# Kernel tuning notes

Hardware: AMD Instinct MI355X
Metric: run time of the kernel (lower is better)

The kernel has to match this reference:

```python
import jax, jax.numpy as jnp
import numpy as np

B, S, H, NH = 2, 2048, 1024, 16
DH = H // NH  # 64

def setup_inputs() -> dict:
    key = jax.random.key(0)
    ks = jax.random.split(key, 6)
    return {
        "hidden_states": jax.random.normal(ks[0], (B, S, H), jnp.float32),
        "attention_mask": jnp.zeros((B, 1, 1, S), jnp.float32),  # additive mask (0 = attend)
        "local_attention_mask": jax.random.randint(ks[1], (B, 1, S, S), 0, 2).astype(jnp.int32),
        "gate_outputs": jax.random.uniform(ks[2], (B, NH, S, 1), jnp.float32),
        "Wq": jax.random.normal(ks[3], (H, H), jnp.float32) * 0.02,
        "bq": jnp.zeros((H,), jnp.float32),
        "Wk": jax.random.normal(ks[4], (H, H), jnp.float32) * 0.02,
        "bk": jnp.zeros((H,), jnp.float32),
        "Wv": jax.random.normal(ks[5], (H, H), jnp.float32) * 0.02,
        "bv": jnp.zeros((H,), jnp.float32),
    }

def _heads(x):
    # [B,S,H] -> [B,NH,S,DH]
    return x.reshape(B, S, NH, DH).transpose(0, 2, 1, 3)

def reference(hidden_states, attention_mask, local_attention_mask, gate_outputs, Wq, bq, Wk, bk, Wv, bv):
    q = _heads(hidden_states @ Wq.T + bq)
    k = _heads(hidden_states @ Wk.T + bk)
    v = _heads(hidden_states @ Wv.T + bv)
    scores = jnp.einsum("bhqd,bhkd->bhqk", q, k) / jnp.sqrt(jnp.float32(DH))
    # global branch (additive mask)
    probs_g = jax.nn.softmax(scores + attention_mask, axis=-1)
    ctx_g = jnp.einsum("bhqk,bhkd->bhqd", probs_g, v)
    # local branch: 0/1 mask -> additive -inf mask
    lmask = (1.0 - local_attention_mask.astype(jnp.float32)) * jnp.finfo(jnp.float32).min
    probs_l = jax.nn.softmax(scores + lmask, axis=-1)
    ctx_l = jnp.einsum("bhqk,bhkd->bhqd", probs_l, v)
    ctx = gate_outputs * ctx_l + (1.0 - gate_outputs) * ctx_g  # [B,NH,S,DH]
    return ctx.transpose(0, 2, 1, 3).reshape(B, S, H)
```

## Files before the change

kernel.cpp:

```cpp
#include <hip/hip_runtime.h>
#include <cstdint>
#include <cstddef>

typedef short short8 __attribute__((ext_vector_type(8)));
typedef float floatx4 __attribute__((ext_vector_type(4)));
typedef unsigned short ushort4v __attribute__((ext_vector_type(4)));
typedef unsigned int uintx4 __attribute__((ext_vector_type(4)));

constexpr int B_ = 2, S_ = 2048, H_ = 1024, NH_ = 16, DH_ = 64;
constexpr int K_ = H_;

__device__ __forceinline__ unsigned short f2bf(float f) {
  unsigned u = __float_as_uint(f);
  u += 0x7fffu + ((u >> 16) & 1u);
  return (unsigned short)(u >> 16);
}

__device__ __forceinline__ unsigned cvtpk(float a, float b) {
  unsigned r;
  asm("v_cvt_pk_bf16_f32 %0, %1, %2" : "=v"(r) : "v"(a), "v"(b));
  return r;
}

__global__ __launch_bounds__(256) void prep_kernel(
    const float* __restrict__ hs, unsigned short* __restrict__ hbf,
    const float* __restrict__ Wq, const float* __restrict__ Wk, const float* __restrict__ Wv,
    unsigned short* __restrict__ wqb, unsigned short* __restrict__ wkb,
    unsigned short* __restrict__ wvb,
    const int* __restrict__ lm, unsigned long long* __restrict__ bm,
    const float* __restrict__ am, float* __restrict__ ea) {
  const int bid = blockIdx.x, tid = threadIdx.x;
  if (bid < 1792) {
    const float* in;
    unsigned short* out;
    int off;
    if (bid < 1024) { in = hs; out = hbf; off = bid; }
    else {
      int wsel = (bid - 1024) >> 8;
      in = (wsel == 0) ? Wq : (wsel == 1) ? Wk : Wv;
      out = (wsel == 0) ? wqb : (wsel == 1) ? wkb : wvb;
      off = (bid - 1024) & 255;
    }
    const int base = off * 4096;
#pragma unroll
    for (int j = 0; j < 4; j++) {
      int i = base + j * 1024 + tid * 4;
      float4 v = *reinterpret_cast<const float4*>(in + i);
      ushort4v o;
      o.x = f2bf(v.x); o.y = f2bf(v.y); o.z = f2bf(v.z); o.w = f2bf(v.w);
      *reinterpret_cast<ushort4v*>(out + i) = o;
    }
  } else if (bid < 9984) {
    const int wbase = (bid - 1792) * 16 + (tid >> 6) * 4;
    const int lane = tid & 63;
#pragma unroll
    for (int j = 0; j < 4; j++) {
      unsigned long long bits = __ballot(lm[(size_t)(wbase + j) * 64 + lane] != 0);
      if (lane == 0) bm[wbase + j] = bits;
    }
  } else {
#pragma unroll
    for (int j = 0; j < 4; j++) {
      int i = j * 1024 + tid * 4;
      float4 v = *reinterpret_cast<const float4*>(am + i);
      float4 o;
      o.x = __expf(v.x); o.y = __expf(v.y); o.z = __expf(v.z); o.w = __expf(v.w);
      *reinterpret_cast<float4*>(ea + i) = o;
    }
  }
}

typedef __attribute__((address_space(1))) const void gvoid;
typedef __attribute__((address_space(3))) void lvoid;
__device__ __forceinline__ void async16(const unsigned short* gp, unsigned short* lp) {
  __builtin_amdgcn_global_load_lds((gvoid*)gp, (lvoid*)lp, 16, 0, 0);
}

__global__ __launch_bounds__(256) void gemm_qkv(
    const unsigned short* __restrict__ A,
    const unsigned short* __restrict__ Wq, const unsigned short* __restrict__ Wk,
    const unsigned short* __restrict__ Wv,
    const float* __restrict__ bq, const float* __restrict__ bk, const float* __restrict__ bv,
    unsigned short* __restrict__ qo, unsigned short* __restrict__ ko,
    unsigned short* __restrict__ vo) {
  __shared__ alignas(16) unsigned short As[2][128 * 32];
  __shared__ alignas(16) unsigned short Bs[2][128 * 32];
  const int z = blockIdx.z;
  const unsigned short* W = (z == 0) ? Wq : (z == 1) ? Wk : Wv;
  const float* bias = (z == 0) ? bq : (z == 1) ? bk : bv;

  const int m0 = blockIdx.x * 128, n0 = blockIdx.y * 128;
  const int tid = threadIdx.x, lane = tid & 63, wvi = tid >> 6;
  const int wr = wvi >> 1, wc = wvi & 1, quad = lane >> 4, l16 = lane & 15;

  floatx4 zf = {0.f, 0.f, 0.f, 0.f};
  floatx4 acc[4][4];
  for (int i = 0; i < 4; i++)
    for (int j = 0; j < 4; j++) acc[i][j] = zf;

  const int cb0 = wvi * 128;
  const int cb1 = wvi * 128 + 64;
  const int c0 = cb0 + lane, c1 = cb1 + lane;
  const unsigned short* As0 = A + (size_t)(m0 + (c0 >> 2)) * K_ + (c0 & 3) * 8;
  const unsigned short* As1 = A + (size_t)(m0 + (c1 >> 2)) * K_ + (c1 & 3) * 8;
  const unsigned short* Ws0 = W + (size_t)(n0 + (c0 >> 2)) * K_ + (c0 & 3) * 8;
  const unsigned short* Ws1 = W + (size_t)(n0 + (c1 >> 2)) * K_ + (c1 & 3) * 8;

  async16(As0, &As[0][cb0 * 8]);
  async16(Ws0, &Bs[0][cb0 * 8]);
  async16(As1, &As[0][cb1 * 8]);
  async16(Ws1, &Bs[0][cb1 * 8]);
  __syncthreads();

  for (int kt = 0; kt < 32; kt++) {
    if (kt != 31) {
      const int kk = (kt + 1) * 32;
      const int bn = (kt + 1) & 1;
      async16(As0 + kk, &As[bn][cb0 * 8]);
      async16(Ws0 + kk, &Bs[bn][cb0 * 8]);
      async16(As1 + kk, &As[bn][cb1 * 8]);
      async16(Ws1 + kk, &Bs[bn][cb1 * 8]);
    }
    const unsigned short* Ah = As[kt & 1];
    const unsigned short* Bh = Bs[kt & 1];
    short8 af[4], bfr[4];
#pragma unroll
    for (int mf = 0; mf < 4; mf++)
      af[mf] = *reinterpret_cast<const short8*>(&Ah[(wr * 64 + mf * 16 + l16) * 32 + quad * 8]);
#pragma unroll
    for (int nf = 0; nf < 4; nf++)
      bfr[nf] = *reinterpret_cast<const short8*>(&Bh[(wc * 64 + nf * 16 + l16) * 32 + quad * 8]);
    if (z == 2) {
#pragma unroll
      for (int mf = 0; mf < 4; mf++)
#pragma unroll
        for (int nf = 0; nf < 4; nf++)
          acc[mf][nf] = __builtin_amdgcn_mfma_f32_16x16x32_bf16(af[mf], bfr[nf], acc[mf][nf], 0, 0, 0);
    } else {
#pragma unroll
      for (int mf = 0; mf < 4; mf++)
#pragma unroll
        for (int nf = 0; nf < 4; nf++)
          acc[mf][nf] = __builtin_amdgcn_mfma_f32_16x16x32_bf16(bfr[nf], af[mf], acc[mf][nf], 0, 0, 0);
    }
    __syncthreads();
  }

  if (z == 2) {
#pragma unroll
    for (int mf = 0; mf < 4; mf++) {
      int mbase = m0 + wr * 64 + mf * 16 + quad * 4;
      int b = mbase >> 11, s0 = mbase & 2047;
      int kl = s0 & 63;
#pragma unroll
      for (int nf = 0; nf < 4; nf++) {
        int n = n0 + wc * 64 + nf * 16 + l16;
        int h = n >> 6, d = n & 63;
        int bh = b * NH_ + h;
        float bvv = bias[n];
        floatx4 c = acc[mf][nf];
        size_t base = (size_t)bh * 131072 + (s0 >> 6) * 4096 + (d >> 4) * 1024 +
                      (kl >> 5) * 512 + ((kl >> 3) & 3) * 128 + (d & 15) * 8 + (kl & 7);
        ushort4v p;
        p.x = f2bf(c[0] + bvv); p.y = f2bf(c[1] + bvv);
        p.z = f2bf(c[2] + bvv); p.w = f2bf(c[3] + bvv);
        *reinterpret_cast<ushort4v*>(&vo[base]) = p;
      }
    }
  } else {
#pragma unroll
    for (int mf = 0; mf < 4; mf++) {
      int s = m0 + wr * 64 + mf * 16 + l16;
      int b = s >> 11;
      int sq = s & 2047;
#pragma unroll
      for (int nf = 0; nf < 4; nf++) {
        int nn = n0 + wc * 64 + nf * 16 + quad * 4;
        int h = nn >> 6, dh = nn & 63;
        int bh = b * NH_ + h;
        float4 b4 = *reinterpret_cast<const float4*>(bias + nn);
        floatx4 c = acc[mf][nf];
        if (z == 0) {
          ushort4v p;
          p.x = f2bf((c[0] + b4.x) * 0.18033688011112042f);
          p.y = f2bf((c[1] + b4.y) * 0.18033688011112042f);
          p.z = f2bf((c[2] + b4.z) * 0.18033688011112042f);
          p.w = f2bf((c[3] + b4.w) * 0.18033688011112042f);
          *reinterpret_cast<ushort4v*>(&qo[((size_t)bh * S_ + sq) * DH_ + dh]) = p;
        } else {
          int kl = sq & 63;
          int t = ((kl >> 4) & 2) | ((kl >> 2) & 1);
          int rr = ((kl >> 1) & 12) | (kl & 3);
          size_t base = (size_t)bh * 131072 + (sq >> 6) * 4096 + t * 1024 +
                        (dh >> 5) * 512 + ((dh >> 3) & 3) * 128 + rr * 8 + (dh & 7);
          ushort4v p;
          p.x = f2bf(c[0] + b4.x); p.y = f2bf(c[1] + b4.y);
          p.z = f2bf(c[2] + b4.z); p.w = f2bf(c[3] + b4.w);
          *reinterpret_cast<ushort4v*>(&ko[base]) = p;
        }
      }
    }
  }
}

__global__ __launch_bounds__(256, 4) void attn_kernel(
    const unsigned short* __restrict__ q,
    const unsigned short* __restrict__ kperm,
    const unsigned short* __restrict__ vperm,
    const float* __restrict__ eam,
    const unsigned long long* __restrict__ bm,
    const float* __restrict__ gate,
    float* __restrict__ out) {
  __shared__ alignas(16) unsigned short Ks[2][4096];
  __shared__ alignas(16) unsigned short Vs[2][4096];

  const int flat = blockIdx.x;
  const int h = (flat & 7) + 8 * ((flat >> 3) & 1);
  const int b = (flat >> 4) & 1;
  const int qt = flat >> 5;
  const int tid = threadIdx.x, lane = tid & 63, wvi = tid >> 6;
  const int quad = lane >> 4, l16 = lane & 15;
  const int bh = b * NH_ + h;
  const int q0 = qt * 64 + wvi * 16;
  const int quad8 = quad * 8;

  const unsigned short* qrow = q + ((size_t)bh * S_ + q0 + l16) * DH_;
  short8 qf0 = *reinterpret_cast<const short8*>(qrow + quad * 8);
  short8 qf1 = *reinterpret_cast<const short8*>(qrow + 32 + quad * 8);

  floatx4 zf = {0.f, 0.f, 0.f, 0.f};
  float psg = 0.f, psl = 0.f;
  floatx4 accg[4], accl[4];
#pragma unroll
  for (int i = 0; i < 4; i++) { accg[i] = zf; accl[i] = zf; }

  const unsigned short* kp = kperm + (size_t)bh * 131072;
  const unsigned short* vp = vperm + (size_t)bh * 131072;
  const float* eamb = eam + (size_t)b * S_;
  const unsigned long long* bmq = bm + ((size_t)b * S_ + q0 + l16) * (S_ / 64);

  const int soA = tid * 8, soB = 2048 + tid * 8;
  const unsigned short* kgA = kp + soA;
  const unsigned short* kgB = kp + soB;
  const unsigned short* vgA = vp + soA;
  const unsigned short* vgB = vp + soB;

  uint4 pk0 = *reinterpret_cast<const uint4*>(kgA);
  uint4 pk1 = *reinterpret_cast<const uint4*>(kgB);
  uint4 pv0 = *reinterpret_cast<const uint4*>(vgA);
  uint4 pv1 = *reinterpret_cast<const uint4*>(vgB);
  *reinterpret_cast<uint4*>(&Ks[0][soA]) = pk0;
  *reinterpret_cast<uint4*>(&Ks[0][soB]) = pk1;
  *reinterpret_cast<uint4*>(&Vs[0][soA]) = pv0;
  *reinterpret_cast<uint4*>(&Vs[0][soB]) = pv1;
  pk0 = *reinterpret_cast<const uint4*>(kgA + 4096);
  pk1 = *reinterpret_cast<const uint4*>(kgB + 4096);
  pv0 = *reinterpret_cast<const uint4*>(vgA + 4096);
  pv1 = *reinterpret_cast<const uint4*>(vgB + 4096);

  for (int kt = 0; kt < S_ / 64; kt++) {
    __syncthreads();
    {
      const int bn = (kt + 1) & 1;
      *reinterpret_cast<uint4*>(&Ks[bn][soA]) = pk0;
      *reinterpret_cast<uint4*>(&Ks[bn][soB]) = pk1;
      *reinterpret_cast<uint4*>(&Vs[bn][soA]) = pv0;
      *reinterpret_cast<uint4*>(&Vs[bn][soB]) = pv1;
    }
    {
      const int tb = ((kt + 2) & 31) * 4096;
      pk0 = *reinterpret_cast<const uint4*>(kgA + tb);
      pk1 = *reinterpret_cast<const uint4*>(kgB + tb);
      pv0 = *reinterpret_cast<const uint4*>(vgA + tb);
      pv1 = *reinterpret_cast<const uint4*>(vgB + tb);
    }
    const int k0 = kt * 64;
    uint2 wv = *reinterpret_cast<const uint2*>(&bmq[kt]);
    unsigned wq0 = wv.x >> quad8;
    unsigned wq1 = wv.y >> quad8;
    float4 ea0 = *reinterpret_cast<const float4*>(eamb + k0 + quad8);
    float4 ea1 = *reinterpret_cast<const float4*>(eamb + k0 + 4 + quad8);
    float4 ea2 = *reinterpret_cast<const float4*>(eamb + k0 + 32 + quad8);
    float4 ea3 = *reinterpret_cast<const float4*>(eamb + k0 + 36 + quad8);

    const unsigned short* Kc = Ks[kt & 1];
    const unsigned short* Vc = Vs[kt & 1];
    floatx4 scT[4];
#pragma unroll
    for (int t = 0; t < 4; t++) {
      const unsigned short* kr = Kc + t * 1024 + lane * 8;
      short8 kf0 = *reinterpret_cast<const short8*>(kr);
      short8 kf1 = *reinterpret_cast<const short8*>(kr + 512);
      scT[t] = __builtin_amdgcn_mfma_f32_16x16x32_bf16(kf0, qf0, zf, 0, 0, 0);
      scT[t] = __builtin_amdgcn_mfma_f32_16x16x32_bf16(kf1, qf1, scT[t], 0, 0, 0);
    }
    uintx4 fgv[2], flv[2];
#pragma unroll
    for (int t = 0; t < 4; t++) {
      const int T = t >> 1, tau = t & 1;
      floatx4 sc = scT[t];
      unsigned wq = T ? wq1 : wq0;
      float4 ea = (t == 0) ? ea0 : (t == 1) ? ea1 : (t == 2) ? ea2 : ea3;
      unsigned m4 = (wq >> (tau * 4)) & 0xFu;
      float e0 = __builtin_amdgcn_exp2f(sc[0]);
      float e1 = __builtin_amdgcn_exp2f(sc[1]);
      float e2 = __builtin_amdgcn_exp2f(sc[2]);
      float e3 = __builtin_amdgcn_exp2f(sc[3]);
      float g0 = e0 * ea.x, g1 = e1 * ea.y, g2 = e2 * ea.z, g3 = e3 * ea.w;
      psg += (g0 + g1) + (g2 + g3);
      float l0 = (m4 & 1u) ? e0 : 0.f;
      float l1 = (m4 & 2u) ? e1 : 0.f;
      float l2 = (m4 & 4u) ? e2 : 0.f;
      float l3 = (m4 & 8u) ? e3 : 0.f;
      psl += (l0 + l1) + (l2 + l3);
      fgv[T][tau * 2]     = cvtpk(g0, g1);
      fgv[T][tau * 2 + 1] = cvtpk(g2, g3);
      flv[T][tau * 2]     = cvtpk(l0, l1);
      flv[T][tau * 2 + 1] = cvtpk(l2, l3);
    }
    short8 FG0 = __builtin_bit_cast(short8, fgv[0]);
    short8 FG1 = __builtin_bit_cast(short8, fgv[1]);
    short8 FL0 = __builtin_bit_cast(short8, flv[0]);
    short8 FL1 = __builtin_bit_cast(short8, flv[1]);
#pragma unroll
    for (int d = 0; d < 4; d++) {
      const unsigned short* vb = Vc + d * 1024 + lane * 8;
      short8 v0 = *reinterpret_cast<const short8*>(vb);
      short8 v1 = *reinterpret_cast<const short8*>(vb + 512);
      accg[d] = __builtin_amdgcn_mfma_f32_16x16x32_bf16(v0, FG0, accg[d], 0, 0, 0);
      accl[d] = __builtin_amdgcn_mfma_f32_16x16x32_bf16(v0, FL0, accl[d], 0, 0, 0);
      accg[d] = __builtin_amdgcn_mfma_f32_16x16x32_bf16(v1, FG1, accg[d], 0, 0, 0);
      accl[d] = __builtin_amdgcn_mfma_f32_16x16x32_bf16(v1, FL1, accl[d], 0, 0, 0);
    }
  }

  float lgf = psg;
  lgf += __shfl_xor(lgf, 16, 64);
  lgf += __shfl_xor(lgf, 32, 64);
  float llf = psl;
  llf += __shfl_xor(llf, 16, 64);
  llf += __shfl_xor(llf, 32, 64);
  const int s = q0 + l16;
  const float g = gate[(size_t)bh * S_ + s];
  const float cg = (1.f - g) / lgf, cl = g / llf;
  float* orow = out + ((size_t)b * S_ + s) * H_ + h * DH_ + quad * 4;
#pragma unroll
  for (int d = 0; d < 4; d++) {
    float4 o;
    o.x = cl * accl[d][0] + cg * accg[d][0];
    o.y = cl * accl[d][1] + cg * accg[d][1];
    o.z = cl * accl[d][2] + cg * accg[d][2];
    o.w = cl * accl[d][3] + cg * accg[d][3];
    *reinterpret_cast<float4*>(orow + d * 16) = o;
  }
}

extern "C" void kernel_launch(void* const* d_in, const int* in_sizes, int n_in,
                              void* d_out, int out_size, void* d_ws, size_t ws_size,
                              hipStream_t stream) {
  (void)in_sizes; (void)n_in; (void)out_size; (void)ws_size;
  const float* hs = (const float*)d_in[0];
  const float* am = (const float*)d_in[1];
  const int* lm = (const int*)d_in[2];
  const float* gate = (const float*)d_in[3];
  const float* Wq = (const float*)d_in[4];
  const float* bq = (const float*)d_in[5];
  const float* Wk = (const float*)d_in[6];
  const float* bk = (const float*)d_in[7];
  const float* Wv = (const float*)d_in[8];
  const float* bv = (const float*)d_in[9];
  float* out = (float*)d_out;

  unsigned short* ws = (unsigned short*)d_ws;
  unsigned short* hbf = ws;
  unsigned short* wqb = hbf + 4194304;
  unsigned short* wkb = wqb + 1048576;
  unsigned short* wvb = wkb + 1048576;
  unsigned short* qb = wvb + 1048576;
  unsigned short* kb = qb + 4194304;
  unsigned short* vtb = kb + 4194304;
  unsigned long long* bmp = (unsigned long long*)(vtb + 4194304);
  float* eamp = (float*)(bmp + 131072);

  prep_kernel<<<9985, 256, 0, stream>>>(hs, hbf, Wq, Wk, Wv, wqb, wkb, wvb, lm, bmp, am, eamp);
  gemm_qkv<<<dim3(32, 8, 3), 256, 0, stream>>>(hbf, wqb, wkb, wvb, bq, bk, bv, qb, kb, vtb);
  attn_kernel<<<dim3(1024), 256, 0, stream>>>(qb, kb, vtb, eamp, bmp, gate, out);
}
```

Baseline: 234.5 us.

## Fuse fp32-to-bf16 conversion into QKV GEMM tile loads

Removes the separate bf16 conversion pass over hidden states and weights from the prep kernel. The GEMM now loads fp32 tiles directly into registers, converts them with packed bf16 instructions, and writes them to LDS, prefetching two tiles ahead in a register-staged pipeline instead of using async global-to-LDS loads. This drops a full write and re-read of the bf16 copies. In exchange the GEMM reads twice as many bytes per tile, each tile is converted by every block that uses it, and register pressure goes up.

```diff
diff --git a/kernel.cpp b/kernel.cpp
--- a/kernel.cpp
+++ b/kernel.cpp
@@ -23,35 +23,11 @@
 }
 
 __global__ __launch_bounds__(256) void prep_kernel(
-    const float* __restrict__ hs, unsigned short* __restrict__ hbf,
-    const float* __restrict__ Wq, const float* __restrict__ Wk, const float* __restrict__ Wv,
-    unsigned short* __restrict__ wqb, unsigned short* __restrict__ wkb,
-    unsigned short* __restrict__ wvb,
     const int* __restrict__ lm, unsigned long long* __restrict__ bm,
     const float* __restrict__ am, float* __restrict__ ea) {
   const int bid = blockIdx.x, tid = threadIdx.x;
-  if (bid < 1792) {
-    const float* in;
-    unsigned short* out;
-    int off;
-    if (bid < 1024) { in = hs; out = hbf; off = bid; }
-    else {
-      int wsel = (bid - 1024) >> 8;
-      in = (wsel == 0) ? Wq : (wsel == 1) ? Wk : Wv;
-      out = (wsel == 0) ? wqb : (wsel == 1) ? wkb : wvb;
-      off = (bid - 1024) & 255;
-    }
-    const int base = off * 4096;
-#pragma unroll
-    for (int j = 0; j < 4; j++) {
-      int i = base + j * 1024 + tid * 4;
-      float4 v = *reinterpret_cast<const float4*>(in + i);
-      ushort4v o;
-      o.x = f2bf(v.x); o.y = f2bf(v.y); o.z = f2bf(v.z); o.w = f2bf(v.w);
-      *reinterpret_cast<ushort4v*>(out + i) = o;
-    }
-  } else if (bid < 9984) {
-    const int wbase = (bid - 1792) * 16 + (tid >> 6) * 4;
+  if (bid < 8192) {
+    const int wbase = bid * 16 + (tid >> 6) * 4;
     const int lane = tid & 63;
 #pragma unroll
     for (int j = 0; j < 4; j++) {
@@ -70,23 +46,17 @@
   }
 }
 
-typedef __attribute__((address_space(1))) const void gvoid;
-typedef __attribute__((address_space(3))) void lvoid;
-__device__ __forceinline__ void async16(const unsigned short* gp, unsigned short* lp) {
-  __builtin_amdgcn_global_load_lds((gvoid*)gp, (lvoid*)lp, 16, 0, 0);
-}
-
 __global__ __launch_bounds__(256) void gemm_qkv(
-    const unsigned short* __restrict__ A,
-    const unsigned short* __restrict__ Wq, const unsigned short* __restrict__ Wk,
-    const unsigned short* __restrict__ Wv,
+    const float* __restrict__ A,
+    const float* __restrict__ Wq, const float* __restrict__ Wk,
+    const float* __restrict__ Wv,
     const float* __restrict__ bq, const float* __restrict__ bk, const float* __restrict__ bv,
     unsigned short* __restrict__ qo, unsigned short* __restrict__ ko,
     unsigned short* __restrict__ vo) {
   __shared__ alignas(16) unsigned short As[2][128 * 32];
   __shared__ alignas(16) unsigned short Bs[2][128 * 32];
   const int z = blockIdx.z;
-  const unsigned short* W = (z == 0) ? Wq : (z == 1) ? Wk : Wv;
+  const float* W = (z == 0) ? Wq : (z == 1) ? Wk : Wv;
   const float* bias = (z == 0) ? bq : (z == 1) ? bk : bv;
 
   const int m0 = blockIdx.x * 128, n0 = blockIdx.y * 128;
@@ -98,29 +68,48 @@
   for (int i = 0; i < 4; i++)
     for (int j = 0; j < 4; j++) acc[i][j] = zf;
 
-  const int cb0 = wvi * 128;
-  const int cb1 = wvi * 128 + 64;
+  const int cb0 = wvi * 128, cb1 = wvi * 128 + 64;
   const int c0 = cb0 + lane, c1 = cb1 + lane;
-  const unsigned short* As0 = A + (size_t)(m0 + (c0 >> 2)) * K_ + (c0 & 3) * 8;
-  const unsigned short* As1 = A + (size_t)(m0 + (c1 >> 2)) * K_ + (c1 & 3) * 8;
-  const unsigned short* Ws0 = W + (size_t)(n0 + (c0 >> 2)) * K_ + (c0 & 3) * 8;
-  const unsigned short* Ws1 = W + (size_t)(n0 + (c1 >> 2)) * K_ + (c1 & 3) * 8;
-
-  async16(As0, &As[0][cb0 * 8]);
-  async16(Ws0, &Bs[0][cb0 * 8]);
-  async16(As1, &As[0][cb1 * 8]);
-  async16(Ws1, &Bs[0][cb1 * 8]);
-  __syncthreads();
+  const float* Ag0 = A + (size_t)(m0 + (c0 >> 2)) * K_ + (c0 & 3) * 8;
+  const float* Ag1 = A + (size_t)(m0 + (c1 >> 2)) * K_ + (c1 & 3) * 8;
+  const float* Wg0 = W + (size_t)(n0 + (c0 >> 2)) * K_ + (c0 & 3) * 8;
+  const float* Wg1 = W + (size_t)(n0 + (c1 >> 2)) * K_ + (c1 & 3) * 8;
+
+  float4 a00, a01, a10, a11, w00, w01, w10, w11;
+  auto LOAD = [&](int t) {
+    const int kk = t * 32;
+    a00 = *reinterpret_cast<const float4*>(Ag0 + kk);
+    a01 = *reinterpret_cast<const float4*>(Ag0 + kk + 4);
+    a10 = *reinterpret_cast<const float4*>(Ag1 + kk);
+    a11 = *reinterpret_cast<const float4*>(Ag1 + kk + 4);
+    w00 = *reinterpret_cast<const float4*>(Wg0 + kk);
+    w01 = *reinterpret_cast<const float4*>(Wg0 + kk + 4);
+    w10 = *reinterpret_cast<const float4*>(Wg1 + kk);
+    w11 = *reinterpret_cast<const float4*>(Wg1 + kk + 4);
+  };
+  auto WRITE = [&](int bn) {
+    uintx4 pa0 = {cvtpk(a00.x, a00.y), cvtpk(a00.z, a00.w),
+                  cvtpk(a01.x, a01.y), cvtpk(a01.z, a01.w)};
+    uintx4 pa1 = {cvtpk(a10.x, a10.y), cvtpk(a10.z, a10.w),
+                  cvtpk(a11.x, a11.y), cvtpk(a11.z, a11.w)};
+    uintx4 pw0 = {cvtpk(w00.x, w00.y), cvtpk(w00.z, w00.w),
+                  cvtpk(w01.x, w01.y), cvtpk(w01.z, w01.w)};
+    uintx4 pw1 = {cvtpk(w10.x, w10.y), cvtpk(w10.z, w10.w),
+                  cvtpk(w11.x, w11.y), cvtpk(w11.z, w11.w)};
+    *reinterpret_cast<uintx4*>(&As[bn][c0 * 8]) = pa0;
+    *reinterpret_cast<uintx4*>(&As[bn][c1 * 8]) = pa1;
+    *reinterpret_cast<uintx4*>(&Bs[bn][c0 * 8]) = pw0;
+    *reinterpret_cast<uintx4*>(&Bs[bn][c1 * 8]) = pw1;
+  };
+
+  LOAD(0);
+  WRITE(0);
+  LOAD(1);
 
   for (int kt = 0; kt < 32; kt++) {
-    if (kt != 31) {
-      const int kk = (kt + 1) * 32;
-      const int bn = (kt + 1) & 1;
-      async16(As0 + kk, &As[bn][cb0 * 8]);
-      async16(Ws0 + kk, &Bs[bn][cb0 * 8]);
-      async16(As1 + kk, &As[bn][cb1 * 8]);
-      async16(Ws1 + kk, &Bs[bn][cb1 * 8]);
-    }
+    __syncthreads();
+    if (kt != 31) WRITE((kt + 1) & 1);
+    if (kt < 30) LOAD(kt + 2);
     const unsigned short* Ah = As[kt & 1];
     const unsigned short* Bh = Bs[kt & 1];
     short8 af[4], bfr[4];
@@ -143,7 +132,6 @@
         for (int nf = 0; nf < 4; nf++)
           acc[mf][nf] = __builtin_amdgcn_mfma_f32_16x16x32_bf16(bfr[nf], af[mf], acc[mf][nf], 0, 0, 0);
     }
-    __syncthreads();
   }
 
   if (z == 2) {
@@ -372,17 +360,13 @@
   float* out = (float*)d_out;
 
   unsigned short* ws = (unsigned short*)d_ws;
-  unsigned short* hbf = ws;
-  unsigned short* wqb = hbf + 4194304;
-  unsigned short* wkb = wqb + 1048576;
-  unsigned short* wvb = wkb + 1048576;
-  unsigned short* qb = wvb + 1048576;
+  unsigned short* qb = ws;
   unsigned short* kb = qb + 4194304;
   unsigned short* vtb = kb + 4194304;
   unsigned long long* bmp = (unsigned long long*)(vtb + 4194304);
   float* eamp = (float*)(bmp + 131072);
 
-  prep_kernel<<<9985, 256, 0, stream>>>(hs, hbf, Wq, Wk, Wv, wqb, wkb, wvb, lm, bmp, am, eamp);
-  gemm_qkv<<<dim3(32, 8, 3), 256, 0, stream>>>(hbf, wqb, wkb, wvb, bq, bk, bv, qb, kb, vtb);
+  prep_kernel<<<8193, 256, 0, stream>>>(lm, bmp, am, eamp);
+  gemm_qkv<<<dim3(32, 8, 3), 256, 0, stream>>>(hs, Wq, Wk, Wv, bq, bk, bv, qb, kb, vtb);
   attn_kernel<<<dim3(1024), 256, 0, stream>>>(qb, kb, vtb, eamp, bmp, gate, out);
 }
```

Result: slower. 242.2 us (+3.3%).
